# Kernel optimization log

Measured on AMD Instinct MI355X. Metric: run time of the kernel, lower is better.

## Reference

```python
import jax, jax.numpy as jnp
import numpy as np

H = 56; W = 56; WS = 7; NW = WS * WS  # 49 tokens per window
HEADS = 8; DIM = 256; HIDDEN = 4 * DIM
SHIFT = NW // 2  # gilbert shift = 24 (shift_size > 0)
SCALE = (DIM // HEADS) ** -0.5
EPS = 1e-5


def _sgn(v):
    return -1 if v < 0 else 1 if v > 0 else 0


def _generate2d(x, y, ax, ay, bx, by, result):
    w = abs(ax + ay); h = abs(bx + by)
    dax, day = _sgn(ax), _sgn(ay); dbx, dby = _sgn(bx), _sgn(by)
    if h == 1 or w == 1:
        if h == 1:
            for _ in range(w):
                result.append((x, y)); x, y = x + dax, y + day
        elif w == 1:
            for _ in range(h):
                result.append((x, y)); x, y = x + dbx, y + dby
        return
    ax2, ay2 = ax // 2, ay // 2; bx2, by2 = bx // 2, by // 2
    w2 = abs(ax2 + ay2); h2 = abs(bx2 + by2)
    if 2 * w > 3 * h:
        if w2 % 2 and w > 2:
            ax2, ay2 = ax2 + dax, ay2 + day
        _generate2d(x, y, ax2, ay2, bx, by, result)
        _generate2d(x + ax2, y + ay2, ax - ax2, ay - ay2, bx, by, result)
    else:
        if h2 % 2 and h > 2:
            bx2, by2 = bx2 + dbx, by2 + dby
        _generate2d(x, y, bx2, by2, ax2, ay2, result)
        _generate2d(x + bx2, y + by2, ax, ay, bx - bx2, by - by2, result)
        _generate2d(x + (ax - dax) + (bx2 - dbx), y + (ay - day) + (by2 - dby),
                    -bx2, -by2, -(ax - ax2), -(ay - ay2), result)


def _gilbert2d(width, height):
    result = []
    if width >= height:
        _generate2d(0, 0, width, 0, 0, height, result)
    else:
        _generate2d(0, 0, 0, height, width, 0, result)
    return result


def _make_rel_index():
    # reverse_map[idx] = (y, x) for gilbert position idx
    path = _gilbert2d(W, H)
    rev = np.zeros((H * W, 2), dtype=np.int64)
    for i, (px, py) in enumerate(path[:H * W]):
        rev[i, 0] = py; rev[i, 1] = px
    pos = np.roll(rev, SHIFT, axis=0)  # shifted block: roll positions by ws^2//2
    n_windows = (H * W) // NW
    pos = pos[:n_windows * NW].reshape(n_windows, NW, 2)
    dh = pos[:, :, 0][:, :, None] - pos[:, :, 0][:, None, :] + (H - 1)
    dw = pos[:, :, 1][:, :, None] - pos[:, :, 1][:, None, :] + (W - 1)
    return (dh * (2 * W - 1) + dw).astype(np.int32)  # (nW, 49, 49)


def setup_inputs() -> dict:
    key = jax.random.key(0)
    ks = jax.random.split(key, 8)
    B, L, C = 32, H * W, DIM
    return {
        "x": jax.random.normal(ks[0], (B, L, C), jnp.float32),
        "qkv_w": jax.random.normal(ks[1], (C, 3 * C), jnp.float32) * 0.02,
        "qkv_b": jnp.zeros((3 * C,), jnp.float32),
        "proj_w": jax.random.normal(ks[2], (C, C), jnp.float32) * 0.02,
        "proj_b": jnp.zeros((C,), jnp.float32),
        "bias_table": jax.random.normal(ks[3], ((2 * H - 1) * (2 * W - 1), HEADS), jnp.float32) * 0.02,
        "norm1_w": jnp.ones((C,), jnp.float32),
        "norm1_b": jnp.zeros((C,), jnp.float32),
        "norm2_w": jnp.ones((C,), jnp.float32),
        "norm2_b": jnp.zeros((C,), jnp.float32),
        "fc1_w": jax.random.normal(ks[4], (C, HIDDEN), jnp.float32) * 0.02,
        "fc1_b": jnp.zeros((HIDDEN,), jnp.float32),
        "fc2_w": jax.random.normal(ks[5], (HIDDEN, C), jnp.float32) * 0.02,
        "fc2_b": jnp.zeros((C,), jnp.float32),
        "rel_index": jnp.asarray(_make_rel_index()),
    }


def _layernorm(x, w, b):
    mu = jnp.mean(x, axis=-1, keepdims=True)
    var = jnp.mean(jnp.square(x - mu), axis=-1, keepdims=True)
    return (x - mu) * jax.lax.rsqrt(var + EPS) * w + b


def reference(x, qkv_w, qkv_b, proj_w, proj_b, bias_table,
              norm1_w, norm1_b, norm2_w, norm2_b,
              fc1_w, fc1_b, fc2_w, fc2_b, rel_index):
    B, L, C = x.shape
    n_win = L // NW
    hd = C // HEADS

    shortcut = x
    h = _layernorm(x, norm1_w, norm1_b)
    # gilbert forward shift along the curve, then window partition
    h = jnp.roll(h, SHIFT, axis=1)
    hw = h.reshape(B * n_win, NW, C)

    qkv = (hw @ qkv_w + qkv_b).reshape(B * n_win, NW, 3, HEADS, hd)
    qkv = jnp.transpose(qkv, (2, 0, 3, 1, 4))  # (3, B*nW, heads, N, hd)
    q, k, v = qkv[0] * SCALE, qkv[1], qkv[2]

    attn = jnp.einsum('bhnd,bhmd->bhnm', q, k)  # (B*nW, heads, 49, 49)
    bias = jnp.transpose(bias_table[rel_index], (0, 3, 1, 2))  # (nW, heads, 49, 49)
    attn = attn.reshape(B, n_win, HEADS, NW, NW) + bias[None]
    attn = jax.nn.softmax(attn, axis=-1).reshape(B * n_win, HEADS, NW, NW)

    out = jnp.einsum('bhnm,bhmd->bhnd', attn, v)
    out = jnp.transpose(out, (0, 2, 1, 3)).reshape(B * n_win, NW, C)
    out = out @ proj_w + proj_b

    # window merge + gilbert reverse shift
    out = out.reshape(B, L, C)
    out = jnp.roll(out, -SHIFT, axis=1)

    x = shortcut + out
    h2 = _layernorm(x, norm2_w, norm2_b)
    h2 = jax.nn.gelu(h2 @ fc1_w + fc1_b, approximate=False) @ fc2_w + fc2_b
    return x + h2
```

## Files before the change

kernel.cpp:

```cpp
#include <hip/hip_runtime.h>
#include <math.h>

typedef unsigned short u16;
typedef __attribute__((ext_vector_type(8))) short bfrag;
typedef __attribute__((ext_vector_type(4))) float f32x4;
typedef __attribute__((ext_vector_type(4))) unsigned short us4;

#define B_SZ 32
#define L_SZ 3136
#define C_SZ 256
#define NHEADS 8
#define HID_SZ 1024
#define NW 49
#define NWIN 64
#define SHIFT 24
#define M_SZ (B_SZ * L_SZ)
#define SCALEF 0.17677669529663687f

__device__ __forceinline__ float bf2f(u16 u) {
  union { unsigned int i; float f; } v; v.i = ((unsigned)u) << 16; return v.f;
}
__device__ __forceinline__ u16 f2bf(float f) {
  union { unsigned int i; float f; } v; v.f = f;
  return (u16)((v.i + 0x7fffu + ((v.i >> 16) & 1u)) >> 16);
}
__device__ __forceinline__ void gload_lds16(const u16* g, u16* l) {
  __builtin_amdgcn_global_load_lds(
      (const __attribute__((address_space(1))) unsigned int*)g,
      (__attribute__((address_space(3))) unsigned int*)l, 16, 0, 0);
}

__global__ void transpose_kernel(const float* __restrict__ in, u16* __restrict__ out,
                                 int K, int N) {
  const int idx = blockIdx.x * 256 + threadIdx.x;
  if (idx >= K * N) return;
  const int n = idx / K;
  const int k = idx - n * K;
  out[idx] = f2bf(in[(size_t)k * N + n]);
}

__global__ void bias_kernel(const float* __restrict__ tab, const int* __restrict__ rel,
                            float* __restrict__ bm) {
  const int idx = blockIdx.x * 256 + threadIdx.x;
  const int tot = NWIN * NHEADS * NW * NW;
  if (idx >= tot) return;
  const int w = idx / (NHEADS * NW * NW);
  const int r = idx - w * (NHEADS * NW * NW);
  const int h = r / (NW * NW);
  const int ij = r - h * (NW * NW);
  bm[idx] = tab[(size_t)rel[w * NW * NW + ij] * NHEADS + h];
}

__global__ __launch_bounds__(256) void ln1_kernel(
    const float* __restrict__ x, const float* __restrict__ w,
    const float* __restrict__ b, u16* __restrict__ out) {
  const int wv = threadIdx.x >> 6;
  const int lane = threadIdx.x & 63;
  const int row0 = blockIdx.x * 16 + wv * 4;
  float4 u[4];
#pragma unroll
  for (int r = 0; r < 4; ++r)
    u[r] = *((const float4*)x + (size_t)(row0 + r) * 64 + lane);
  float s[4], sq[4];
#pragma unroll
  for (int r = 0; r < 4; ++r) {
    s[r]  = u[r].x + u[r].y + u[r].z + u[r].w;
    sq[r] = u[r].x * u[r].x + u[r].y * u[r].y + u[r].z * u[r].z + u[r].w * u[r].w;
  }
#pragma unroll
  for (int d = 1; d < 64; d <<= 1)
#pragma unroll
    for (int r = 0; r < 4; ++r) {
      s[r] += __shfl_xor(s[r], d); sq[r] += __shfl_xor(sq[r], d);
    }
  float wv4[4], bv4[4];
#pragma unroll
  for (int j = 0; j < 4; ++j) { wv4[j] = w[lane * 4 + j]; bv4[j] = b[lane * 4 + j]; }
#pragma unroll
  for (int r = 0; r < 4; ++r) {
    const int row = row0 + r;
    const float mu = s[r] * (1.0f / C_SZ);
    const float rs = rsqrtf(sq[r] * (1.0f / C_SZ) - mu * mu + 1e-5f);
    const int bb = row / L_SZ;
    int l2 = row - bb * L_SZ + SHIFT;
    if (l2 >= L_SZ) l2 -= L_SZ;
    const float vv[4] = {u[r].x, u[r].y, u[r].z, u[r].w};
    us4 ov;
#pragma unroll
    for (int j = 0; j < 4; ++j) ov[j] = f2bf((vv[j] - mu) * rs * wv4[j] + bv4[j]);
    *(us4*)(out + ((size_t)bb * L_SZ + l2) * C_SZ + lane * 4) = ov;
  }
}

__global__ __launch_bounds__(256) void ln2_kernel(
    const u16* __restrict__ x, const float* __restrict__ w,
    const float* __restrict__ b, u16* __restrict__ out) {
  const int wv = threadIdx.x >> 6;
  const int lane = threadIdx.x & 63;
  const int row0 = blockIdx.x * 16 + wv * 4;
  us4 u[4];
#pragma unroll
  for (int r = 0; r < 4; ++r)
    u[r] = *(const us4*)(x + (size_t)(row0 + r) * C_SZ + lane * 4);
  float v[4][4], s[4], sq[4];
#pragma unroll
  for (int r = 0; r < 4; ++r) {
    s[r] = 0.f; sq[r] = 0.f;
#pragma unroll
    for (int j = 0; j < 4; ++j) {
      v[r][j] = bf2f(u[r][j]); s[r] += v[r][j]; sq[r] += v[r][j] * v[r][j];
    }
  }
#pragma unroll
  for (int d = 1; d < 64; d <<= 1)
#pragma unroll
    for (int r = 0; r < 4; ++r) {
      s[r] += __shfl_xor(s[r], d); sq[r] += __shfl_xor(sq[r], d);
    }
  float wv4[4], bv4[4];
#pragma unroll
  for (int j = 0; j < 4; ++j) { wv4[j] = w[lane * 4 + j]; bv4[j] = b[lane * 4 + j]; }
#pragma unroll
  for (int r = 0; r < 4; ++r) {
    const float mu = s[r] * (1.0f / C_SZ);
    const float rs = rsqrtf(sq[r] * (1.0f / C_SZ) - mu * mu + 1e-5f);
    us4 ov;
#pragma unroll
    for (int j = 0; j < 4; ++j) ov[j] = f2bf((v[r][j] - mu) * rs * wv4[j] + bv4[j]);
    *(us4*)(out + (size_t)(row0 + r) * C_SZ + lane * 4) = ov;
  }
}

#define BM 128
#define BN 128
#define BKT 64

template <int MODE>
__global__ __launch_bounds__(256, 2) void gemm_kernel(
    const u16* __restrict__ A, const u16* __restrict__ Bt,
    const float* __restrict__ bias, int N, int K, void* __restrict__ Cout,
    const float* __restrict__ resx, const u16* __restrict__ resb2) {
  __shared__ u16 Als[BM * BKT];
  __shared__ u16 Bls[BN * BKT];
  const int nbx = N / BN;
  const int per = gridDim.x >> 3;
  const int lin = (blockIdx.x & 7) * per + (blockIdx.x >> 3);
  const int by = lin / nbx;
  const int bx = lin - by * nbx;
  const int m0 = by * BM;
  const int n0 = bx * BN;

  const int tid = threadIdx.x;
  const int lane = tid & 63;
  const int lr = lane & 15;
  const int lg = lane >> 4;
  const int wid = tid >> 6;
  const int wm = (wid >> 1) * 64;
  const int wn = (wid & 1) * 64;

  const int grow = lane >> 3;
  const int gch = (lane & 7) ^ grow;

  const f32x4 fzero = {0.f, 0.f, 0.f, 0.f};
  f32x4 acc[4][4];
#pragma unroll
  for (int i = 0; i < 4; ++i)
#pragma unroll
    for (int j = 0; j < 4; ++j) acc[i][j] = fzero;

  const u16* Agl = A + (size_t)m0 * K + gch * 8;
  const u16* Bgl = Bt + (size_t)n0 * K + gch * 8;

  for (int k0 = 0; k0 < K; k0 += BKT) {
#pragma unroll
    for (int g = 0; g < 4; ++g) {
      const int rbase = wid * 32 + g * 8;
      gload_lds16(Agl + (size_t)(rbase + grow) * K + k0, Als + rbase * 64);
      gload_lds16(Bgl + (size_t)(rbase + grow) * K + k0, Bls + rbase * 64);
    }
    __syncthreads();
#pragma unroll
    for (int s = 0; s < 2; ++s) {
      const int kg = s * 4 + lg;
      bfrag af[4], bfv[4];
#pragma unroll
      for (int m = 0; m < 4; ++m) {
        const int r = wm + m * 16 + lr;
        af[m] = *(const bfrag*)(Als + r * 64 + ((kg ^ (r & 7)) * 8));
      }
#pragma unroll
      for (int n = 0; n < 4; ++n) {
        const int r = wn + n * 16 + lr;
        bfv[n] = *(const bfrag*)(Bls + r * 64 + ((kg ^ (r & 7)) * 8));
      }
#pragma unroll
      for (int m = 0; m < 4; ++m)
#pragma unroll
        for (int n = 0; n < 4; ++n)
          acc[m][n] = __builtin_amdgcn_mfma_f32_16x16x32_bf16(af[m], bfv[n],
                                                              acc[m][n], 0, 0, 0);
    }
    __syncthreads();
  }

  float bv4[4];
#pragma unroll
  for (int n = 0; n < 4; ++n) bv4[n] = bias[n0 + wn + n * 16 + lr];

#pragma unroll
  for (int m = 0; m < 4; ++m) {
#pragma unroll
    for (int i = 0; i < 4; ++i) {
      const int row = m0 + wm + m * 16 + lg * 4 + i;
      if (MODE == 1) {
        const int bb = row / L_SZ;
        int l2 = row - bb * L_SZ - SHIFT;
        if (l2 < 0) l2 += L_SZ;
        const size_t orow = (size_t)bb * L_SZ + l2;
#pragma unroll
        for (int n = 0; n < 4; ++n) {
          const int col = n0 + wn + n * 16 + lr;
          ((u16*)Cout)[orow * N + col] =
              f2bf(resx[orow * N + col] + acc[m][n][i] + bv4[n]);
        }
      } else if (MODE == 2) {
#pragma unroll
        for (int n = 0; n < 4; ++n) {
          const int col = n0 + wn + n * 16 + lr;
          float v = acc[m][n][i] + bv4[n];
          v = 0.5f * v * (1.0f + erff(v * 0.70710678f));
          ((u16*)Cout)[(size_t)row * N + col] = f2bf(v);
        }
      } else if (MODE == 3) {
#pragma unroll
        for (int n = 0; n < 4; ++n) {
          const int col = n0 + wn + n * 16 + lr;
          ((float*)Cout)[(size_t)row * N + col] =
              acc[m][n][i] + bv4[n] + bf2f(resb2[(size_t)row * N + col]);
        }
      } else {
#pragma unroll
        for (int n = 0; n < 4; ++n) {
          const int col = n0 + wn + n * 16 + lr;
          ((u16*)Cout)[(size_t)row * N + col] = f2bf(acc[m][n][i] + bv4[n]);
        }
      }
    }
  }
}

__global__ __launch_bounds__(256) void attn_kernel(const u16* __restrict__ qkv,
                                                   const float* __restrict__ bm,
                                                   u16* __restrict__ out) {
  __shared__ u16 Pls[4][64 * 72];
  __shared__ u16 Vls[4][64 * 32];
  const int widx = blockIdx.x >> 1;
  const int half = blockIdx.x & 1;
  const int w = widx & (NWIN - 1);
  const int wv = threadIdx.x >> 6;
  const int lane = threadIdx.x & 63;
  const int lr = lane & 15;
  const int lg = lane >> 4;
  const size_t base = (size_t)widx * NW;
  u16* P = Pls[wv];
  u16* Vl = Vls[wv];
  const f32x4 fzero = {0.f, 0.f, 0.f, 0.f};
  const int h = half * 4 + wv;

#pragma unroll
  for (int g = 0; g < 4; ++g) {
    int row = g * 16 + (lane >> 2);
    if (row > NW - 1) row = NW - 1;
    const int sc = (lane & 3) ^ ((row ^ (row >> 2)) & 3);
    gload_lds16(qkv + (base + row) * 768 + 512 + h * 32 + sc * 8, Vl + g * 512);
  }

  bfrag qf[4], kf[4];
#pragma unroll
  for (int m = 0; m < 4; ++m) {
    int r = m * 16 + lr; if (r > NW - 1) r = NW - 1;
    qf[m] = *(const bfrag*)(qkv + (base + r) * 768 + h * 32 + lg * 8);
    kf[m] = *(const bfrag*)(qkv + (base + r) * 768 + 256 + h * 32 + lg * 8);
  }
  f32x4 s[4][4];
#pragma unroll
  for (int m = 0; m < 4; ++m)
#pragma unroll
    for (int n = 0; n < 4; ++n)
      s[m][n] = __builtin_amdgcn_mfma_f32_16x16x32_bf16(qf[m], kf[n], fzero, 0, 0, 0);

  const float* bh = bm + (size_t)(w * NHEADS + h) * (NW * NW);
#pragma unroll
  for (int m = 0; m < 4; ++m) {
#pragma unroll
    for (int i = 0; i < 4; ++i) {
      const int row = m * 16 + lg * 4 + i;
      const int brow = row > NW - 1 ? NW - 1 : row;
      float vals[4];
#pragma unroll
      for (int n = 0; n < 4; ++n) {
        const int c = n * 16 + lr;
        vals[n] = (c < NW) ? (s[m][n][i] * SCALEF + bh[brow * NW + c]) : -1e30f;
      }
      float mx = fmaxf(fmaxf(vals[0], vals[1]), fmaxf(vals[2], vals[3]));
#pragma unroll
      for (int d = 1; d < 16; d <<= 1) mx = fmaxf(mx, __shfl_xor(mx, d));
      float sum = 0.f;
#pragma unroll
      for (int n = 0; n < 4; ++n) { vals[n] = __expf(vals[n] - mx); sum += vals[n]; }
#pragma unroll
      for (int d = 1; d < 16; d <<= 1) sum += __shfl_xor(sum, d);
      const float inv = 1.0f / sum;
#pragma unroll
      for (int n = 0; n < 4; ++n)
        P[row * 72 + n * 16 + lr] = f2bf(vals[n] * inv);
    }
  }
  asm volatile("s_waitcnt vmcnt(0)" ::: "memory");
  f32x4 o[4][2];
#pragma unroll
  for (int m = 0; m < 4; ++m) { o[m][0] = fzero; o[m][1] = fzero; }
#pragma unroll
  for (int s2 = 0; s2 < 2; ++s2) {
    bfrag pf[4], vf[2];
#pragma unroll
    for (int m = 0; m < 4; ++m)
      pf[m] = *(const bfrag*)(P + (m * 16 + lr) * 72 + s2 * 32 + lg * 8);
#pragma unroll
    for (int n = 0; n < 2; ++n) {
      const int d = n * 16 + lr;
      const int cd = d >> 3;
#pragma unroll
      for (int i = 0; i < 8; ++i) {
        const int kk = s2 * 32 + lg * 8 + i;
        const int slot = cd ^ ((kk ^ (kk >> 2)) & 3);
        vf[n][i] = *(const short*)(Vl + kk * 32 + slot * 8 + (d & 7));
      }
    }
#pragma unroll
    for (int m = 0; m < 4; ++m)
#pragma unroll
      for (int n = 0; n < 2; ++n)
        o[m][n] = __builtin_amdgcn_mfma_f32_16x16x32_bf16(pf[m], vf[n],
                                                          o[m][n], 0, 0, 0);
  }
#pragma unroll
  for (int m = 0; m < 4; ++m)
#pragma unroll
    for (int i = 0; i < 4; ++i) {
      const int row = m * 16 + lg * 4 + i;
      if (row < NW) {
#pragma unroll
        for (int n = 0; n < 2; ++n)
          out[(base + row) * C_SZ + h * 32 + n * 16 + lr] = f2bf(o[m][n][i]);
      }
    }
}

extern "C" void kernel_launch(void* const* d_in, const int* in_sizes, int n_in,
                              void* d_out, int out_size, void* d_ws, size_t ws_size,
                              hipStream_t stream) {
  (void)in_sizes; (void)n_in; (void)out_size;
  const float* x     = (const float*)d_in[0];
  const float* qkvw  = (const float*)d_in[1];
  const float* qkvb  = (const float*)d_in[2];
  const float* projw = (const float*)d_in[3];
  const float* projb = (const float*)d_in[4];
  const float* btab  = (const float*)d_in[5];
  const float* n1w   = (const float*)d_in[6];
  const float* n1b   = (const float*)d_in[7];
  const float* n2w   = (const float*)d_in[8];
  const float* n2b   = (const float*)d_in[9];
  const float* fc1w  = (const float*)d_in[10];
  const float* fc1b  = (const float*)d_in[11];
  const float* fc2w  = (const float*)d_in[12];
  const float* fc2b  = (const float*)d_in[13];
  const int* rel     = (const int*)d_in[14];

  char* ws = (char*)d_ws;
  size_t off = 0;
  auto alloc = [&](size_t bytes) -> char* {
    char* p = ws + off; off += (bytes + 255) & ~(size_t)255; return p;
  };
  u16* qkvwT   = (u16*)alloc((size_t)768 * 256 * 2);
  u16* projwT  = (u16*)alloc((size_t)256 * 256 * 2);
  u16* fc1wT   = (u16*)alloc((size_t)1024 * 256 * 2);
  u16* fc2wT   = (u16*)alloc((size_t)256 * 1024 * 2);
  float* biasm = (float*)alloc((size_t)NWIN * NHEADS * NW * NW * 4);
  u16* bufh    = (u16*)alloc((size_t)M_SZ * C_SZ * 2);
  u16* x2b     = (u16*)alloc((size_t)M_SZ * C_SZ * 2);

  char* tail = ws + off;
  u16* qkvbuf   = (u16*)tail;
  u16* scratch2 = (u16*)tail;
  const size_t full_scr = (size_t)M_SZ * HID_SZ * 2;
  const int nch = (ws_size >= off + full_scr) ? 1 : 4;
  const int mch = M_SZ / nch;

  transpose_kernel<<<(256 * 768 + 255) / 256, 256, 0, stream>>>(qkvw, qkvwT, 256, 768);
  transpose_kernel<<<(256 * 256 + 255) / 256, 256, 0, stream>>>(projw, projwT, 256, 256);
  transpose_kernel<<<(256 * 1024 + 255) / 256, 256, 0, stream>>>(fc1w, fc1wT, 256, 1024);
  transpose_kernel<<<(1024 * 256 + 255) / 256, 256, 0, stream>>>(fc2w, fc2wT, 1024, 256);
  bias_kernel<<<(NWIN * NHEADS * NW * NW + 255) / 256, 256, 0, stream>>>(btab, rel, biasm);

  ln1_kernel<<<M_SZ / 16, 256, 0, stream>>>(x, n1w, n1b, bufh);

  gemm_kernel<0><<<(768 / BN) * (M_SZ / BM), 256, 0, stream>>>(
      bufh, qkvwT, qkvb, 768, 256, qkvbuf, nullptr, nullptr);

  attn_kernel<<<B_SZ * NWIN * 2, 256, 0, stream>>>(qkvbuf, biasm, bufh);

  gemm_kernel<1><<<(256 / BN) * (M_SZ / BM), 256, 0, stream>>>(
      bufh, projwT, projb, 256, 256, x2b, x, nullptr);

  for (int q = 0; q < nch; ++q) {
    const size_t roff = (size_t)q * mch;
    ln2_kernel<<<mch / 16, 256, 0, stream>>>(x2b + roff * C_SZ, n2w, n2b,
                                             bufh + roff * C_SZ);
    gemm_kernel<2><<<(HID_SZ / BN) * (mch / BM), 256, 0, stream>>>(
        bufh + roff * C_SZ, fc1wT, fc1b, 1024, 256, scratch2, nullptr, nullptr);
    gemm_kernel<3><<<(256 / BN) * (mch / BM), 256, 0, stream>>>(
        scratch2, fc2wT, fc2b, 256, 1024, (float*)d_out + roff * C_SZ,
        nullptr, x2b + roff * C_SZ);
  }
}
```

Before: 456.8 us.

## Chunk QKV GEMM and attention into four passes; always chunk MLP; raise GEMM occupancy

```diff
diff --git a/kernel.cpp b/kernel.cpp
--- a/kernel.cpp
+++ b/kernel.cpp
@@ -15,6 +15,9 @@
 #define NWIN 64
 #define SHIFT 24
 #define M_SZ (B_SZ * L_SZ)
+#define NCH 4
+#define MCH (M_SZ / NCH)
+#define WCH (B_SZ * NWIN / NCH)
 #define SCALEF 0.17677669529663687f
 
 __device__ __forceinline__ float bf2f(u16 u) {
@@ -136,7 +139,7 @@
 #define BKT 64
 
 template <int MODE>
-__global__ __launch_bounds__(256, 2) void gemm_kernel(
+__global__ __launch_bounds__(256, 4) void gemm_kernel(
     const u16* __restrict__ A, const u16* __restrict__ Bt,
     const float* __restrict__ bias, int N, int K, void* __restrict__ Cout,
     const float* __restrict__ resx, const u16* __restrict__ resb2) {
@@ -251,17 +254,17 @@
 
 __global__ __launch_bounds__(256) void attn_kernel(const u16* __restrict__ qkv,
                                                    const float* __restrict__ bm,
-                                                   u16* __restrict__ out) {
+                                                   u16* __restrict__ out, int widx0) {
   __shared__ u16 Pls[4][64 * 72];
   __shared__ u16 Vls[4][64 * 32];
-  const int widx = blockIdx.x >> 1;
+  const int wl = blockIdx.x >> 1;
   const int half = blockIdx.x & 1;
-  const int w = widx & (NWIN - 1);
+  const int w = (widx0 + wl) & (NWIN - 1);
   const int wv = threadIdx.x >> 6;
   const int lane = threadIdx.x & 63;
   const int lr = lane & 15;
   const int lg = lane >> 4;
-  const size_t base = (size_t)widx * NW;
+  const size_t base = (size_t)wl * NW;
   u16* P = Pls[wv];
   u16* Vl = Vls[wv];
   const f32x4 fzero = {0.f, 0.f, 0.f, 0.f};
@@ -360,7 +363,7 @@
 extern "C" void kernel_launch(void* const* d_in, const int* in_sizes, int n_in,
                               void* d_out, int out_size, void* d_ws, size_t ws_size,
                               hipStream_t stream) {
-  (void)in_sizes; (void)n_in; (void)out_size;
+  (void)in_sizes; (void)n_in; (void)out_size; (void)ws_size;
   const float* x     = (const float*)d_in[0];
   const float* qkvw  = (const float*)d_in[1];
   const float* qkvb  = (const float*)d_in[2];
@@ -389,13 +392,9 @@
   float* biasm = (float*)alloc((size_t)NWIN * NHEADS * NW * NW * 4);
   u16* bufh    = (u16*)alloc((size_t)M_SZ * C_SZ * 2);
   u16* x2b     = (u16*)alloc((size_t)M_SZ * C_SZ * 2);
-
   char* tail = ws + off;
   u16* qkvbuf   = (u16*)tail;
   u16* scratch2 = (u16*)tail;
-  const size_t full_scr = (size_t)M_SZ * HID_SZ * 2;
-  const int nch = (ws_size >= off + full_scr) ? 1 : 4;
-  const int mch = M_SZ / nch;
 
   transpose_kernel<<<(256 * 768 + 255) / 256, 256, 0, stream>>>(qkvw, qkvwT, 256, 768);
   transpose_kernel<<<(256 * 256 + 255) / 256, 256, 0, stream>>>(projw, projwT, 256, 256);
@@ -405,21 +404,24 @@
 
   ln1_kernel<<<M_SZ / 16, 256, 0, stream>>>(x, n1w, n1b, bufh);
 
-  gemm_kernel<0><<<(768 / BN) * (M_SZ / BM), 256, 0, stream>>>(
-      bufh, qkvwT, qkvb, 768, 256, qkvbuf, nullptr, nullptr);
-
-  attn_kernel<<<B_SZ * NWIN * 2, 256, 0, stream>>>(qkvbuf, biasm, bufh);
+  for (int c = 0; c < NCH; ++c) {
+    const size_t roff = (size_t)c * MCH;
+    gemm_kernel<0><<<(768 / BN) * (MCH / BM), 256, 0, stream>>>(
+        bufh + roff * C_SZ, qkvwT, qkvb, 768, 256, qkvbuf, nullptr, nullptr);
+    attn_kernel<<<WCH * 2, 256, 0, stream>>>(qkvbuf, biasm, bufh + roff * C_SZ,
+                                             c * WCH);
+  }
 
   gemm_kernel<1><<<(256 / BN) * (M_SZ / BM), 256, 0, stream>>>(
       bufh, projwT, projb, 256, 256, x2b, x, nullptr);
 
-  for (int q = 0; q < nch; ++q) {
-    const size_t roff = (size_t)q * mch;
-    ln2_kernel<<<mch / 16, 256, 0, stream>>>(x2b + roff * C_SZ, n2w, n2b,
+  for (int q = 0; q < NCH; ++q) {
+    const size_t roff = (size_t)q * MCH;
+    ln2_kernel<<<MCH / 16, 256, 0, stream>>>(x2b + roff * C_SZ, n2w, n2b,
                                              bufh + roff * C_SZ);
-    gemm_kernel<2><<<(HID_SZ / BN) * (mch / BM), 256, 0, stream>>>(
+    gemm_kernel<2><<<(HID_SZ / BN) * (MCH / BM), 256, 0, stream>>>(
         bufh + roff * C_SZ, fc1wT, fc1b, 1024, 256, scratch2, nullptr, nullptr);
-    gemm_kernel<3><<<(256 / BN) * (mch / BM), 256, 0, stream>>>(
+    gemm_kernel<3><<<(256 / BN) * (MCH / BM), 256, 0, stream>>>(
         scratch2, fc2wT, fc2b, 256, 1024, (float*)d_out + roff * C_SZ,
         nullptr, x2b + roff * C_SZ);
   }
```

Result: slower. 521.7 us (+14.2%).
